# Kernel optimization log

Hardware: AMD Instinct MI355X
Metric: run time of the kernel (lower is better)

Reference implementation:

```python
import jax, jax.numpy as jnp
import numpy as np

NUM_IMU = 72
NUM_NOISE = 12
MAX_PROP = 300
LN_EPS = 1e-5

def _softplus(x):
    return jax.nn.softplus(x)

def setup_inputs() -> dict:
    key = jax.random.key(0)
    k1, k2, k3, k4, k5 = jax.random.split(key, 5)
    d_model = 1024
    seq_len = 4096
    hidden_states = jax.random.normal(k1, (1, seq_len, d_model), dtype=jnp.float32)
    ln_gamma = jnp.ones((d_model,), dtype=jnp.float32)
    ln_beta = jnp.zeros((d_model,), dtype=jnp.float32)
    # Linear: d_model -> NUM_IMU * NUM_NOISE
    W = jax.random.normal(k2, (d_model, NUM_IMU * NUM_NOISE), dtype=jnp.float32) / np.sqrt(d_model)
    b = jax.random.normal(k3, (NUM_IMU * NUM_NOISE,), dtype=jnp.float32) * 0.01
    return {"hidden_states": hidden_states, "ln_gamma": ln_gamma, "ln_beta": ln_beta, "W": W, "b": b}

def _forward(hidden_states, ln_gamma, ln_beta, W, b):
    seq_len = hidden_states.shape[1]
    tsteps = min(MAX_PROP, seq_len)
    x = hidden_states[0]  # [seq, d_model] (squeeze batch=1)
    mu = jnp.mean(x, axis=-1, keepdims=True)
    var = jnp.mean((x - mu) ** 2, axis=-1, keepdims=True)
    xn = (x - mu) * jax.lax.rsqrt(var + LN_EPS) * ln_gamma + ln_beta
    # noise params: [seq, NUM_NOISE, NUM_IMU]
    p = (xn @ W + b).reshape(seq_len, NUM_NOISE, NUM_IMU)
    c = p[:, 4, :]
    c_theta = p[:, 5, :]
    phi = p[:, 6, :]
    phi_theta = p[:, 7, :]
    d = _softplus(p[:, 1, :])
    k = d ** 2 / 4 + _softplus(p[:, 0, :])
    d_theta = _softplus(p[:, 3, :])
    k_theta = d_theta ** 2 / 4 + _softplus(p[:, 2, :])
    acc_base = p[:, 8, :].T      # [imu, seq]
    acc_std = _softplus(p[:, 9, :]).T
    gyro_base = p[:, 10, :].T
    gyro_std = _softplus(p[:, 11, :]).T
    # vectorize over imu: move to [imu, seq, 1]
    def I(a):
        return a.T[:, :, None]
    t = jnp.arange(tsteps, dtype=jnp.float32)[None, None, :]  # [1,1,tstep]
    k_, d_, phi_, c_ = I(k), I(d), I(phi), I(c)
    kt_, dt_, pht_, ct_ = I(k_theta), I(d_theta), I(phi_theta), I(c_theta)
    omega1 = jnp.sqrt(k_ * 4 - d_ ** 2) / 2
    lin = c_ * jnp.exp(-d_ / 2 * t) * jnp.sin(t * omega1 + phi_)
    omega2 = jnp.sqrt(kt_ * 4 - dt_ ** 2) / 2
    ang = ct_ * jnp.exp(-dt_ / 2 * t) * jnp.sin(t * omega2 + pht_)
    spring = lin + ang  # [imu, seq, tstep]
    # banded scatter-add: out[s+t] += spring[:, s, t] for s+t < seq_len
    pos = jnp.arange(seq_len, dtype=jnp.int32)[:, None] + jnp.arange(tsteps, dtype=jnp.int32)[None, :]
    pos_flat = pos.reshape(-1)
    mask = pos_flat < seq_len
    pos_safe = jnp.where(mask, pos_flat, 0)
    vals = spring.reshape(NUM_IMU, -1) * mask.astype(spring.dtype)
    kinematics = jnp.zeros((NUM_IMU, seq_len), dtype=spring.dtype).at[:, pos_safe].add(vals)
    return kinematics, acc_base, acc_std, gyro_base, gyro_std

def reference(hidden_states, ln_gamma, ln_beta, W, b):
    return _forward(hidden_states, ln_gamma, ln_beta, W, b)
```

## Files before the change

### kernel.cpp

```cpp
#include <hip/hip_runtime.h>
#include <hip/hip_bf16.h>
#include <math.h>

#define SEQ 4096
#define DM  1024
#define NIMU 72
#define NNOISE 12
#define NJ (NIMU*NNOISE)
#define TSTEPS 300
#define PLANE (NIMU*SEQ)

#define A2F_SHORTS ((size_t)256 * 64 * 512)
#define BTF_SHORTS ((size_t)56 * 64 * 512)

typedef __attribute__((ext_vector_type(8))) short bf16x8;
typedef __attribute__((ext_vector_type(4))) float f32x4;
typedef __attribute__((ext_vector_type(2))) float f32x2;

__device__ __forceinline__ float softplus_f(float x) {
    return fmaxf(x, 0.f) + log1pf(expf(-fabsf(x)));
}

__device__ __forceinline__ void split_bf16(float x, short& hi, short& lo) {
    unsigned b = __float_as_uint(x);
    unsigned h = (b + 0x7FFFu + ((b >> 16) & 1u)) >> 16;
    float hf = __uint_as_float(h << 16);
    float r = x - hf;
    unsigned b2 = __float_as_uint(r);
    unsigned l2 = (b2 + 0x7FFFu + ((b2 >> 16) & 1u)) >> 16;
    hi = (short)h;
    lo = (short)l2;
}

__global__ __launch_bounds__(256) void ln_kernel(const float* __restrict__ x,
                                                 const float* __restrict__ gamma,
                                                 const float* __restrict__ beta,
                                                 short* __restrict__ A2f) {
    const int s_tile = blockIdx.x;
    const int tid = threadIdx.x;
    const int mrow = tid >> 4;
    const int g    = tid & 15;
    const int row  = s_tile * 16 + mrow;
    const float4* xr = (const float4*)(x + (size_t)row * DM);

    float s = 0.f, sq = 0.f;
    #pragma unroll
    for (int i = 0; i < 16; ++i) {
        float4 v = xr[g + 16 * i];
        s  += v.x + v.y + v.z + v.w;
        sq += v.x*v.x + v.y*v.y + v.z*v.z + v.w*v.w;
    }
    #pragma unroll
    for (int off = 1; off < 16; off <<= 1) {
        s  += __shfl_xor(s, off);
        sq += __shfl_xor(sq, off);
    }
    const float mean = s * (1.f / DM);
    const float var  = sq * (1.f / DM) - mean * mean;
    const float rstd = rsqrtf(fmaxf(var, 0.f) + 1e-5f);

    #pragma unroll
    for (int i = 0; i < 16; ++i) {
        float4 v = xr[g + 16 * i];
        float4 gm = ((const float4*)gamma)[g + 16 * i];
        float4 bt = ((const float4*)beta)[g + 16 * i];
        float o[4];
        o[0] = (v.x - mean) * rstd * gm.x + bt.x;
        o[1] = (v.y - mean) * rstd * gm.y + bt.y;
        o[2] = (v.z - mean) * rstd * gm.z + bt.z;
        o[3] = (v.w - mean) * rstd * gm.w + bt.w;
        short4 hv, lv;
        split_bf16(o[0], hv.x, lv.x);
        split_bf16(o[1], hv.y, lv.y);
        split_bf16(o[2], hv.z, lv.z);
        split_bf16(o[3], hv.w, lv.w);
        const int ch = (g >> 3) + 2 * i;
        const size_t base = ((size_t)s_tile * 64 + ch) * 512
                          + mrow * 8 + ((g >> 1) & 3) * 128 + (g & 1) * 4;
        *(short4*)(A2f + base)             = hv;
        *(short4*)(A2f + base + 32 * 512)  = lv;
    }
}

__global__ __launch_bounds__(256) void wprep_kernel(const float* __restrict__ W,
                                                    short* __restrict__ Btf) {
    __shared__ float T[32][33];
    const int k0 = blockIdx.x * 32, j0 = blockIdx.y * 32;
    const int t = threadIdx.x;
    {
        const int r = t >> 3, c4 = (t & 7) * 4;
        float4 v = *(const float4*)(W + (size_t)(k0 + r) * NJ + j0 + c4);
        T[r][c4 + 0] = v.x; T[r][c4 + 1] = v.y; T[r][c4 + 2] = v.z; T[r][c4 + 3] = v.w;
    }
    __syncthreads();
    if (t < 128) {
        const int gq = t >> 6;
        const int l  = t & 63;
        const int n = l & 15, c = l >> 4;
        const int jt = blockIdx.y * 2 + gq;
        bf16x8 hv, lv;
        #pragma unroll
        for (int o = 0; o < 8; ++o) {
            short h, lo_;
            split_bf16(T[c * 8 + o][gq * 16 + n], h, lo_);
            hv[o] = h; lv[o] = lo_;
        }
        short* dh = Btf + ((size_t)jt * 64 + blockIdx.x) * 512 + l * 8;
        *(bf16x8*)dh = hv;
        *(bf16x8*)(dh + (size_t)32 * 512) = lv;
    }
}

__global__ __launch_bounds__(256, 1) void gemm_kernel(const short* __restrict__ A2f,
                                                      const short* __restrict__ Btf,
                                                      const float* __restrict__ bias,
                                                      float* __restrict__ pt,
                                                      float* __restrict__ out) {
    const int l = threadIdx.x & 63, w = threadIdx.x >> 6;
    const int st0 = blockIdx.x * 8 + (w & 1) * 4;
    const int jt0 = blockIdx.y * 8 + (w >> 1) * 4;
    const short* aB = A2f + (size_t)st0 * (64 * 512) + l * 8;
    const short* bB = Btf + (size_t)jt0 * (64 * 512) + l * 8;

    f32x4 acc[4][4] = {};
    bf16x8 ah[2][4], al[2][4], bh[2][4], bl[2][4];

    auto ldstep = [&](int slot, int i) {
        #pragma unroll
        for (int t = 0; t < 4; ++t) {
            ah[slot][t] = *(const bf16x8*)(aB + ((size_t)t * 64 + i) * 512);
            al[slot][t] = *(const bf16x8*)(aB + ((size_t)t * 64 + 32 + i) * 512);
            bh[slot][t] = *(const bf16x8*)(bB + ((size_t)t * 64 + i) * 512);
            bl[slot][t] = *(const bf16x8*)(bB + ((size_t)t * 64 + 32 + i) * 512);
        }
    };

    ldstep(0, 0);
    #pragma unroll 2
    for (int i = 0; i < 32; ++i) {
        const int cur = i & 1;
        if (i + 1 < 32) ldstep(cur ^ 1, i + 1);
        #pragma unroll
        for (int mi = 0; mi < 4; ++mi)
            #pragma unroll
            for (int ni = 0; ni < 4; ++ni)
                acc[mi][ni] = __builtin_amdgcn_mfma_f32_16x16x32_bf16(
                    ah[cur][mi], bh[cur][ni], acc[mi][ni], 0, 0, 0);
        #pragma unroll
        for (int mi = 0; mi < 4; ++mi)
            #pragma unroll
            for (int ni = 0; ni < 4; ++ni)
                acc[mi][ni] = __builtin_amdgcn_mfma_f32_16x16x32_bf16(
                    ah[cur][mi], bl[cur][ni], acc[mi][ni], 0, 0, 0);
        #pragma unroll
        for (int mi = 0; mi < 4; ++mi)
            #pragma unroll
            for (int ni = 0; ni < 4; ++ni)
                acc[mi][ni] = __builtin_amdgcn_mfma_f32_16x16x32_bf16(
                    al[cur][mi], bh[cur][ni], acc[mi][ni], 0, 0, 0);
    }

    const int srow = (l >> 4) * 4;
    const int jcol = l & 15;
    #pragma unroll
    for (int ni = 0; ni < 4; ++ni) {
        const int j = (jt0 + ni) * 16 + jcol;
        if (j < NJ) {
            const float bj = bias[j];
            if (j < 8 * NIMU) {
                #pragma unroll
                for (int mi = 0; mi < 4; ++mi) {
                    f32x4 v = acc[mi][ni];
                    v[0] += bj; v[1] += bj; v[2] += bj; v[3] += bj;
                    *(f32x4*)(pt + (size_t)j * SEQ + (st0 + mi) * 16 + srow) = v;
                }
            } else {
                const int q  = (j - 8 * NIMU) / NIMU;
                const int im = (j - 8 * NIMU) - NIMU * q;
                float* dst = out + (size_t)(1 + q) * PLANE + (size_t)im * SEQ;
                #pragma unroll
                for (int mi = 0; mi < 4; ++mi) {
                    f32x4 v = acc[mi][ni];
                    v[0] += bj; v[1] += bj; v[2] += bj; v[3] += bj;
                    if (q & 1) {
                        v[0] = softplus_f(v[0]); v[1] = softplus_f(v[1]);
                        v[2] = softplus_f(v[2]); v[3] = softplus_f(v[3]);
                    }
                    *(f32x4*)(dst + (st0 + mi) * 16 + srow) = v;
                }
            }
        }
    }
}

__global__ __launch_bounds__(256) void spring_kernel(const float* __restrict__ pt,
                                                     float* __restrict__ kin) {
    const int lane = threadIdx.x & 63;
    const int wid  = threadIdx.x >> 6;
    const int sblk = blockIdx.x * 4 + wid;
    const int imu  = blockIdx.y;
    const int sbase = sblk * 64;
    const int s    = sbase + lane;

    const int base = imu * SEQ + s;
    const float p0  = pt[(size_t)0 * PLANE + base];
    const float p1  = pt[(size_t)1 * PLANE + base];
    const float p2  = pt[(size_t)2 * PLANE + base];
    const float p3  = pt[(size_t)3 * PLANE + base];
    const float c1  = pt[(size_t)4 * PLANE + base];
    const float c2  = pt[(size_t)5 * PLANE + base];
    const float ph1 = pt[(size_t)6 * PLANE + base];
    const float ph2 = pt[(size_t)7 * PLANE + base];

    float dd = softplus_f(p1);
    float kk = dd * dd * 0.25f + softplus_f(p0);
    float om1 = 0.5f * sqrtf(fmaxf(4.f * kk - dd * dd, 0.f));
    float dt = softplus_f(p3);
    float kt = dt * dt * 0.25f + softplus_f(p2);
    float om2 = 0.5f * sqrtf(fmaxf(4.f * kt - dt * dt, 0.f));
    float e1 = expf(-0.5f * dd), e2 = expf(-0.5f * dt);
    float sn, cs, sn2, cs2;
    sincosf(om1, &sn, &cs);
    sincosf(om2, &sn2, &cs2);
    const f32x2 Rr = {e1 * cs, e2 * cs2};
    const f32x2 Ri = {e1 * sn, e2 * sn2};
    sincosf(ph1, &sn, &cs);
    sincosf(ph2, &sn2, &cs2);
    f32x2 zr = {c1 * cs, c2 * cs2};
    f32x2 zi = {c1 * sn, c2 * sn2};

    float a = 0.f;
    float d = 0.f;
    float* kimu = kin + (size_t)imu * SEQ;

    #pragma unroll
    for (int q = 0; q < 5; ++q) {
        const int steps = (q == 4) ? 44 : 64;
        #pragma unroll
        for (int tr = 0; tr < steps; ++tr) {
            float v = zi.x + zi.y;
            f32x2 nr = zr * Rr - zi * Ri;
            zi = zr * Ri + zi * Rr;
            zr = nr;
            int as = __builtin_amdgcn_update_dpp(0, __float_as_int(a),
                                                 0x130, 0xF, 0xF, true);
            a = __int_as_float(as) + v;
            int u = __builtin_amdgcn_readlane(__float_as_int(a), 0);
            d = (lane == tr) ? __int_as_float(u) : d;
        }
        const int pos = sbase + q * 64 + lane;
        if (pos < SEQ)
            __hip_atomic_fetch_add(kimu + pos, d,
                                   __ATOMIC_RELAXED, __HIP_MEMORY_SCOPE_AGENT);
        d = 0.f;
    }

    if (lane > 0) {
        const int pos = sbase + 299 + lane;
        if (pos < SEQ)
            __hip_atomic_fetch_add(kimu + pos, a,
                                   __ATOMIC_RELAXED, __HIP_MEMORY_SCOPE_AGENT);
    }
}

extern "C" void kernel_launch(void* const* d_in, const int* in_sizes, int n_in,
                              void* d_out, int out_size, void* d_ws, size_t ws_size,
                              hipStream_t stream) {
    const float* hs    = (const float*)d_in[0];
    const float* gamma = (const float*)d_in[1];
    const float* beta  = (const float*)d_in[2];
    const float* W     = (const float*)d_in[3];
    const float* b     = (const float*)d_in[4];
    float* out = (float*)d_out;

    short* A2f = (short*)d_ws;
    short* Btf = A2f + A2F_SHORTS;
    float* pt  = (float*)(Btf + BTF_SHORTS);

    (void)hipMemsetAsync(out, 0, (size_t)PLANE * sizeof(float), stream);

    ln_kernel<<<SEQ / 16, 256, 0, stream>>>(hs, gamma, beta, A2f);
    wprep_kernel<<<dim3(DM / 32, NJ / 32), 256, 0, stream>>>(W, Btf);
    gemm_kernel<<<dim3(SEQ / 128, 7), 256, 0, stream>>>(A2f, Btf, b, pt, out);
    spring_kernel<<<dim3(16, NIMU), 256, 0, stream>>>(pt, out);
}
```

Measured before the change: 163.6 us.

## Switch GEMM to 32x32x16 MFMA with one tile per wave and matching layouts

Replaces the 4x4 grid of 16x16x32 bf16 MFMAs per wave with a single 32x32x16 MFMA tile per wave, and re-lays out the pre-split bf16 hi/lo A and B fragments to match. The LN and W-prep kernels are rewritten to emit the new fragment layout, and the GEMM grid becomes 64x14 blocks with smaller per-wave tiles. The aim is more blocks to fill the CUs and use of the larger MFMA shape. The cost is less register-level reuse per wave, so each wave issues more global loads per MFMA.

Result: slower. 173.3 us (+5.9%).

```diff
diff --git a/kernel.cpp b/kernel.cpp
--- a/kernel.cpp
+++ b/kernel.cpp
@@ -10,12 +10,13 @@
 #define TSTEPS 300
 #define PLANE (NIMU*SEQ)
 
-#define A2F_SHORTS ((size_t)256 * 64 * 512)
-#define BTF_SHORTS ((size_t)56 * 64 * 512)
-
-typedef __attribute__((ext_vector_type(8))) short bf16x8;
-typedef __attribute__((ext_vector_type(4))) float f32x4;
-typedef __attribute__((ext_vector_type(2))) float f32x2;
+#define A2F_SHORTS ((size_t)128 * 128 * 512)
+#define BTF_SHORTS ((size_t)28 * 128 * 512)
+
+typedef __attribute__((ext_vector_type(8)))  short bf16x8;
+typedef __attribute__((ext_vector_type(4)))  float f32x4;
+typedef __attribute__((ext_vector_type(2)))  float f32x2;
+typedef __attribute__((ext_vector_type(16))) float f32x16;
 
 __device__ __forceinline__ float softplus_f(float x) {
     return fmaxf(x, 0.f) + log1pf(expf(-fabsf(x)));
@@ -38,20 +39,20 @@
                                                  short* __restrict__ A2f) {
     const int s_tile = blockIdx.x;
     const int tid = threadIdx.x;
-    const int mrow = tid >> 4;
-    const int g    = tid & 15;
-    const int row  = s_tile * 16 + mrow;
+    const int mrow = tid >> 3;
+    const int g    = tid & 7;
+    const int row  = s_tile * 32 + mrow;
     const float4* xr = (const float4*)(x + (size_t)row * DM);
 
     float s = 0.f, sq = 0.f;
     #pragma unroll
-    for (int i = 0; i < 16; ++i) {
-        float4 v = xr[g + 16 * i];
+    for (int i = 0; i < 32; ++i) {
+        float4 v = xr[g + 8 * i];
         s  += v.x + v.y + v.z + v.w;
         sq += v.x*v.x + v.y*v.y + v.z*v.z + v.w*v.w;
     }
     #pragma unroll
-    for (int off = 1; off < 16; off <<= 1) {
+    for (int off = 1; off < 8; off <<= 1) {
         s  += __shfl_xor(s, off);
         sq += __shfl_xor(sq, off);
     }
@@ -59,11 +60,13 @@
     const float var  = sq * (1.f / DM) - mean * mean;
     const float rstd = rsqrtf(fmaxf(var, 0.f) + 1e-5f);
 
-    #pragma unroll
-    for (int i = 0; i < 16; ++i) {
-        float4 v = xr[g + 16 * i];
-        float4 gm = ((const float4*)gamma)[g + 16 * i];
-        float4 bt = ((const float4*)beta)[g + 16 * i];
+    short* tbase = A2f + (size_t)s_tile * (128 * 512)
+                 + mrow * 8 + ((g >> 1) & 1) * 256 + (g & 1) * 4;
+    #pragma unroll
+    for (int i = 0; i < 32; ++i) {
+        float4 v  = xr[g + 8 * i];
+        float4 gm = ((const float4*)gamma)[g + 8 * i];
+        float4 bt = ((const float4*)beta)[g + 8 * i];
         float o[4];
         o[0] = (v.x - mean) * rstd * gm.x + bt.x;
         o[1] = (v.y - mean) * rstd * gm.y + bt.y;
@@ -74,18 +77,18 @@
         split_bf16(o[1], hv.y, lv.y);
         split_bf16(o[2], hv.z, lv.z);
         split_bf16(o[3], hv.w, lv.w);
-        const int ch = (g >> 3) + 2 * i;
-        const size_t base = ((size_t)s_tile * 64 + ch) * 512
-                          + mrow * 8 + ((g >> 1) & 3) * 128 + (g & 1) * 4;
-        *(short4*)(A2f + base)             = hv;
-        *(short4*)(A2f + base + 32 * 512)  = lv;
+        const int ch = (g >> 2) + 2 * i;
+        *(short4*)(tbase + (size_t)ch * 512)              = hv;
+        *(short4*)(tbase + (size_t)(64 + ch) * 512)       = lv;
     }
 }
 
 __global__ __launch_bounds__(256) void wprep_kernel(const float* __restrict__ W,
                                                     short* __restrict__ Btf) {
     __shared__ float T[32][33];
-    const int k0 = blockIdx.x * 32, j0 = blockIdx.y * 32;
+    const int k0 = blockIdx.x * 32;
+    const int jt = blockIdx.y;
+    const int j0 = jt * 32;
     const int t = threadIdx.x;
     {
         const int r = t >> 3, c4 = (t & 7) * 4;
@@ -93,101 +96,76 @@
         T[r][c4 + 0] = v.x; T[r][c4 + 1] = v.y; T[r][c4 + 2] = v.z; T[r][c4 + 3] = v.w;
     }
     __syncthreads();
-    if (t < 128) {
-        const int gq = t >> 6;
-        const int l  = t & 63;
-        const int n = l & 15, c = l >> 4;
-        const int jt = blockIdx.y * 2 + gq;
-        bf16x8 hv, lv;
-        #pragma unroll
-        for (int o = 0; o < 8; ++o) {
-            short h, lo_;
-            split_bf16(T[c * 8 + o][gq * 16 + n], h, lo_);
-            hv[o] = h; lv[o] = lo_;
-        }
-        short* dh = Btf + ((size_t)jt * 64 + blockIdx.x) * 512 + l * 8;
-        *(bf16x8*)dh = hv;
-        *(bf16x8*)(dh + (size_t)32 * 512) = lv;
-    }
-}
-
-__global__ __launch_bounds__(256, 1) void gemm_kernel(const short* __restrict__ A2f,
-                                                      const short* __restrict__ Btf,
-                                                      const float* __restrict__ bias,
-                                                      float* __restrict__ pt,
-                                                      float* __restrict__ out) {
+    const int quad = t >> 6;
+    const int l    = t & 63;
+    const int hilo = quad >> 1, chl = quad & 1;
+    const int jcol = l & 31, kc = l >> 5;
+    bf16x8 ov;
+    #pragma unroll
+    for (int o = 0; o < 8; ++o) {
+        short h, lo_;
+        split_bf16(T[16 * chl + 8 * kc + o][jcol], h, lo_);
+        ov[o] = hilo ? lo_ : h;
+    }
+    *(bf16x8*)(Btf + ((size_t)jt * 128 + (k0 >> 4) + chl + 64 * hilo) * 512 + l * 8) = ov;
+}
+
+__global__ __launch_bounds__(256) void gemm_kernel(const short* __restrict__ A2f,
+                                                   const short* __restrict__ Btf,
+                                                   const float* __restrict__ bias,
+                                                   float* __restrict__ pt,
+                                                   float* __restrict__ out) {
     const int l = threadIdx.x & 63, w = threadIdx.x >> 6;
-    const int st0 = blockIdx.x * 8 + (w & 1) * 4;
-    const int jt0 = blockIdx.y * 8 + (w >> 1) * 4;
-    const short* aB = A2f + (size_t)st0 * (64 * 512) + l * 8;
-    const short* bB = Btf + (size_t)jt0 * (64 * 512) + l * 8;
-
-    f32x4 acc[4][4] = {};
-    bf16x8 ah[2][4], al[2][4], bh[2][4], bl[2][4];
+    const int st = blockIdx.x * 2 + (w & 1);
+    const int jt = blockIdx.y * 2 + (w >> 1);
+    const short* aB = A2f + (size_t)st * (128 * 512) + l * 8;
+    const short* bB = Btf + (size_t)jt * (128 * 512) + l * 8;
+
+    f32x16 acc = {};
+    bf16x8 ah[2], al[2], bh[2], bl[2];
 
     auto ldstep = [&](int slot, int i) {
-        #pragma unroll
-        for (int t = 0; t < 4; ++t) {
-            ah[slot][t] = *(const bf16x8*)(aB + ((size_t)t * 64 + i) * 512);
-            al[slot][t] = *(const bf16x8*)(aB + ((size_t)t * 64 + 32 + i) * 512);
-            bh[slot][t] = *(const bf16x8*)(bB + ((size_t)t * 64 + i) * 512);
-            bl[slot][t] = *(const bf16x8*)(bB + ((size_t)t * 64 + 32 + i) * 512);
-        }
+        ah[slot] = *(const bf16x8*)(aB + (size_t)i * 512);
+        al[slot] = *(const bf16x8*)(aB + (size_t)(64 + i) * 512);
+        bh[slot] = *(const bf16x8*)(bB + (size_t)i * 512);
+        bl[slot] = *(const bf16x8*)(bB + (size_t)(64 + i) * 512);
     };
 
     ldstep(0, 0);
-    #pragma unroll 2
-    for (int i = 0; i < 32; ++i) {
+    #pragma unroll 4
+    for (int i = 0; i < 64; ++i) {
         const int cur = i & 1;
-        if (i + 1 < 32) ldstep(cur ^ 1, i + 1);
-        #pragma unroll
-        for (int mi = 0; mi < 4; ++mi)
+        if (i + 1 < 64) ldstep(cur ^ 1, i + 1);
+        acc = __builtin_amdgcn_mfma_f32_32x32x16_bf16(ah[cur], bh[cur], acc, 0, 0, 0);
+        acc = __builtin_amdgcn_mfma_f32_32x32x16_bf16(ah[cur], bl[cur], acc, 0, 0, 0);
+        acc = __builtin_amdgcn_mfma_f32_32x32x16_bf16(al[cur], bh[cur], acc, 0, 0, 0);
+    }
+
+    const int j = jt * 32 + (l & 31);
+    if (j < NJ) {
+        const float bj = bias[j];
+        const int sb = st * 32 + 4 * (l >> 5);
+        if (j < 8 * NIMU) {
+            float* dst = pt + (size_t)j * SEQ + sb;
             #pragma unroll
-            for (int ni = 0; ni < 4; ++ni)
-                acc[mi][ni] = __builtin_amdgcn_mfma_f32_16x16x32_bf16(
-                    ah[cur][mi], bh[cur][ni], acc[mi][ni], 0, 0, 0);
-        #pragma unroll
-        for (int mi = 0; mi < 4; ++mi)
+            for (int rg = 0; rg < 4; ++rg) {
+                f32x4 v = {acc[4*rg+0] + bj, acc[4*rg+1] + bj,
+                           acc[4*rg+2] + bj, acc[4*rg+3] + bj};
+                *(f32x4*)(dst + 8 * rg) = v;
+            }
+        } else {
+            const int q  = (j - 8 * NIMU) / NIMU;
+            const int im = (j - 8 * NIMU) - NIMU * q;
+            float* dst = out + (size_t)(1 + q) * PLANE + (size_t)im * SEQ + sb;
             #pragma unroll
-            for (int ni = 0; ni < 4; ++ni)
-                acc[mi][ni] = __builtin_amdgcn_mfma_f32_16x16x32_bf16(
-                    ah[cur][mi], bl[cur][ni], acc[mi][ni], 0, 0, 0);
-        #pragma unroll
-        for (int mi = 0; mi < 4; ++mi)
-            #pragma unroll
-            for (int ni = 0; ni < 4; ++ni)
-                acc[mi][ni] = __builtin_amdgcn_mfma_f32_16x16x32_bf16(
-                    al[cur][mi], bh[cur][ni], acc[mi][ni], 0, 0, 0);
-    }
-
-    const int srow = (l >> 4) * 4;
-    const int jcol = l & 15;
-    #pragma unroll
-    for (int ni = 0; ni < 4; ++ni) {
-        const int j = (jt0 + ni) * 16 + jcol;
-        if (j < NJ) {
-            const float bj = bias[j];
-            if (j < 8 * NIMU) {
-                #pragma unroll
-                for (int mi = 0; mi < 4; ++mi) {
-                    f32x4 v = acc[mi][ni];
-                    v[0] += bj; v[1] += bj; v[2] += bj; v[3] += bj;
-                    *(f32x4*)(pt + (size_t)j * SEQ + (st0 + mi) * 16 + srow) = v;
+            for (int rg = 0; rg < 4; ++rg) {
+                f32x4 v = {acc[4*rg+0] + bj, acc[4*rg+1] + bj,
+                           acc[4*rg+2] + bj, acc[4*rg+3] + bj};
+                if (q & 1) {
+                    v[0] = softplus_f(v[0]); v[1] = softplus_f(v[1]);
+                    v[2] = softplus_f(v[2]); v[3] = softplus_f(v[3]);
                 }
-            } else {
-                const int q  = (j - 8 * NIMU) / NIMU;
-                const int im = (j - 8 * NIMU) - NIMU * q;
-                float* dst = out + (size_t)(1 + q) * PLANE + (size_t)im * SEQ;
-                #pragma unroll
-                for (int mi = 0; mi < 4; ++mi) {
-                    f32x4 v = acc[mi][ni];
-                    v[0] += bj; v[1] += bj; v[2] += bj; v[3] += bj;
-                    if (q & 1) {
-                        v[0] = softplus_f(v[0]); v[1] = softplus_f(v[1]);
-                        v[2] = softplus_f(v[2]); v[3] = softplus_f(v[3]);
-                    }
-                    *(f32x4*)(dst + (st0 + mi) * 16 + srow) = v;
-                }
+                *(f32x4*)(dst + 8 * rg) = v;
             }
         }
     }
@@ -279,8 +257,8 @@
 
     (void)hipMemsetAsync(out, 0, (size_t)PLANE * sizeof(float), stream);
 
-    ln_kernel<<<SEQ / 16, 256, 0, stream>>>(hs, gamma, beta, A2f);
-    wprep_kernel<<<dim3(DM / 32, NJ / 32), 256, 0, stream>>>(W, Btf);
-    gemm_kernel<<<dim3(SEQ / 128, 7), 256, 0, stream>>>(A2f, Btf, b, pt, out);
+    ln_kernel<<<SEQ / 32, 256, 0, stream>>>(hs, gamma, beta, A2f);
+    wprep_kernel<<<dim3(DM / 32, 27), 256, 0, stream>>>(W, Btf);
+    gemm_kernel<<<dim3(64, 14), 256, 0, stream>>>(A2f, Btf, b, pt, out);
     spring_kernel<<<dim3(16, NIMU), 256, 0, stream>>>(pt, out);
 }
```
